# Optimization experiments

Hardware: AMD Instinct MI355X
Metric: run time of the kernel (lower is better)

The kernel has to match this reference:

```python
import jax, jax.numpy as jnp
import numpy as np

N_NODES = 50000
N_EDGES = 800000
D = 256          # node / edge feature dim (hs[-1])
H = 512          # hs[0] == hs[1] == 2*D
LN_EPS = 1e-5


def setup_inputs() -> dict:
    key = jax.random.key(0)
    ks = jax.random.split(key, 8)
    x = jax.random.normal(ks[0], (N_NODES, D), dtype=jnp.float32)
    edge_index = jax.random.randint(ks[1], (2, N_EDGES), 0, N_NODES, dtype=jnp.int64)
    edge_attr = jax.random.normal(ks[2], (N_EDGES, D), dtype=jnp.float32)
    # MLP(hs=[512,512,256]): Linear(512->512) + SiLU, Linear(512->256); then LayerNorm(256)
    s1 = 1.0 / np.sqrt(H)
    s2 = 1.0 / np.sqrt(H)
    W1 = jax.random.uniform(ks[3], (H, H), jnp.float32, -s1, s1)
    b1 = jax.random.uniform(ks[4], (H,), jnp.float32, -s1, s1)
    W2 = jax.random.uniform(ks[5], (H, D), jnp.float32, -s2, s2)
    b2 = jax.random.uniform(ks[6], (D,), jnp.float32, -s2, s2)
    gamma = jnp.ones((D,), jnp.float32)
    beta = jnp.zeros((D,), jnp.float32)
    return {"x": x, "edge_index": edge_index, "edge_attr": edge_attr,
            "W1": W1, "b1": b1, "W2": W2, "b2": b2,
            "gamma": gamma, "beta": beta}


def reference(x, edge_index, edge_attr, W1, b1, W2, b2, gamma, beta):
    i = edge_index[0]  # destination nodes
    # scatter-add edge features onto nodes: [N, D]
    agg = jax.ops.segment_sum(edge_attr, i, num_segments=x.shape[0])
    h = jnp.concatenate([x, agg], axis=-1)            # [N, 2D]
    h = jax.nn.silu(h @ W1 + b1)                      # [N, H]
    h = h @ W2 + b2                                   # [N, D]
    # LayerNorm(D)
    mu = jnp.mean(h, axis=-1, keepdims=True)
    var = jnp.mean(jnp.square(h - mu), axis=-1, keepdims=True)
    h = (h - mu) * jax.lax.rsqrt(var + LN_EPS) * gamma + beta
    return h + x
```

## Files before the change

kernel.cpp:

```cpp
#include <hip/hip_runtime.h>
#include <hip/hip_bf16.h>
#include <math.h>
#include <stdint.h>

typedef __bf16 bf16_t;
typedef __bf16 bf16x4 __attribute__((ext_vector_type(4)));
typedef __bf16 bf16x8 __attribute__((ext_vector_type(8)));
typedef float  f32x4  __attribute__((ext_vector_type(4)));

#define D_FEAT 256
#define H_FEAT 512
#define LN_EPS 1e-5f
#define CAP    96

#define GLOBAL_AS __attribute__((address_space(1)))
#define LDS_AS    __attribute__((address_space(3)))

__global__ __launch_bounds__(256) void wprep_kernel(const float* __restrict__ W1,
                                                    const float* __restrict__ W2,
                                                    bf16_t* __restrict__ W1t,
                                                    bf16_t* __restrict__ W2t,
                                                    int* __restrict__ counts, int n_nodes) {
    __shared__ float tile[32][33];
    int b = blockIdx.x;
    int gtid = b * 256 + threadIdx.x;
    if (gtid < n_nodes) counts[gtid] = 0;

    int tx = threadIdx.x & 31, ty = threadIdx.x >> 5;
    if (b < 256) {
        int k0 = (b >> 4) * 32, n0 = (b & 15) * 32;
#pragma unroll
        for (int j = 0; j < 4; ++j)
            tile[ty * 4 + j][tx] = W1[(size_t)(k0 + ty * 4 + j) * H_FEAT + n0 + tx];
        __syncthreads();
#pragma unroll
        for (int j = 0; j < 4; ++j)
            W1t[(size_t)(n0 + ty * 4 + j) * H_FEAT + k0 + tx] = (bf16_t)tile[tx][ty * 4 + j];
    } else {
        int bb = b - 256;
        int k0 = (bb >> 3) * 32, n0 = (bb & 7) * 32;
#pragma unroll
        for (int j = 0; j < 4; ++j)
            tile[ty * 4 + j][tx] = W2[(size_t)(k0 + ty * 4 + j) * D_FEAT + n0 + tx];
        __syncthreads();
#pragma unroll
        for (int j = 0; j < 4; ++j)
            W2t[(size_t)(n0 + ty * 4 + j) * H_FEAT + k0 + tx] = (bf16_t)tile[tx][ty * 4 + j];
    }
}

__global__ void place_kernel(const int* __restrict__ dst, int* __restrict__ counts,
                             int* __restrict__ sorted_eid, int n_edges) {
    int e = blockIdx.x * blockDim.x + threadIdx.x;
    if (e < n_edges) {
        int d = dst[e];
        int pos = atomicAdd(&counts[d], 1);
        if (pos < CAP) sorted_eid[(long)d * CAP + pos] = e;
    }
}

__global__ __launch_bounds__(256) void gather_kernel(
    const float* __restrict__ edge_attr, const int* __restrict__ sorted_eid,
    const int* __restrict__ counts, const float* __restrict__ x,
    bf16_t* __restrict__ h_in, int n_nodes) {
    int node = (blockIdx.x * blockDim.x + threadIdx.x) >> 6;
    int lane = threadIdx.x & 63;
    if (node >= n_nodes) return;
    int cnt_all = counts[node]; if (cnt_all > CAP) cnt_all = CAP;
    long s = (long)node * CAP;

    f32x4 accA = {0.f, 0.f, 0.f, 0.f};
    f32x4 accB = {0.f, 0.f, 0.f, 0.f};
    for (int b0 = 0; b0 < cnt_all; b0 += 64) {
        int cnt = cnt_all - b0; if (cnt > 64) cnt = 64;
        int eid_l = (b0 + lane < cnt_all) ? sorted_eid[s + b0 + lane] : 0;
        int j = 0;
        for (; j + 4 <= cnt; j += 4) {
            int e0 = __shfl(eid_l, j);
            int e1 = __shfl(eid_l, j + 1);
            int e2 = __shfl(eid_l, j + 2);
            int e3 = __shfl(eid_l, j + 3);
            f32x4 v0 = __builtin_nontemporal_load((const f32x4*)(edge_attr + (long)e0 * D_FEAT + lane * 4));
            f32x4 v1 = __builtin_nontemporal_load((const f32x4*)(edge_attr + (long)e1 * D_FEAT + lane * 4));
            f32x4 v2 = __builtin_nontemporal_load((const f32x4*)(edge_attr + (long)e2 * D_FEAT + lane * 4));
            f32x4 v3 = __builtin_nontemporal_load((const f32x4*)(edge_attr + (long)e3 * D_FEAT + lane * 4));
            accA += v0; accB += v1; accA += v2; accB += v3;
        }
        for (; j < cnt; ++j) {
            int e0 = __shfl(eid_l, j);
            accA += __builtin_nontemporal_load((const f32x4*)(edge_attr + (long)e0 * D_FEAT + lane * 4));
        }
    }
    f32x4 acc = accA + accB;

    const f32x4 xv = *(const f32x4*)(x + (long)node * D_FEAT + lane * 4);
    bf16x4 ox, oa;
#pragma unroll
    for (int i = 0; i < 4; ++i) { ox[i] = (bf16_t)xv[i]; oa[i] = (bf16_t)acc[i]; }
    *(bf16x4*)(h_in + (long)node * H_FEAT + lane * 4) = ox;
    *(bf16x4*)(h_in + (long)node * H_FEAT + D_FEAT + lane * 4) = oa;
}

__global__ __launch_bounds__(256) void gemm1_kernel(
    const bf16_t* __restrict__ h_in, const bf16_t* __restrict__ W1t,
    const float* __restrict__ b1, bf16_t* __restrict__ act, int n_nodes) {
    __shared__ bf16_t As[2][128 * 32];
    __shared__ bf16_t Bs[2][128 * 32];
    int l = threadIdx.x & 63;
    int w = threadIdx.x >> 6;
    int wr = w >> 1, wc = w & 1;
    int browbase = blockIdx.x * 128;
    int bcolbase = blockIdx.y * 128;
    int lr = l & 15;
    int sg = l >> 4;

    f32x4 zero = {0.f, 0.f, 0.f, 0.f};
    f32x4 acc[4][4];
#pragma unroll
    for (int m = 0; m < 4; ++m)
#pragma unroll
        for (int n = 0; n < 4; ++n) acc[m][n] = zero;

    auto stage = [&](int buf, int k0) {
#pragma unroll
        for (int q = 0; q < 2; ++q) {
            int lrow = w * 32 + q * 16 + (l >> 2);
            int ssrc = (l & 3) ^ ((lrow >> 1) & 3);
            int ga = browbase + lrow; if (ga >= n_nodes) ga = 0;
            const bf16_t* gA = h_in + (size_t)ga * H_FEAT + k0 + ssrc * 8;
            bf16_t* lA = &As[buf][(w * 32 + q * 16) * 32];
            __builtin_amdgcn_global_load_lds((const GLOBAL_AS uint32_t*)gA,
                                             (LDS_AS uint32_t*)lA, 16, 0, 0);
            int gb = bcolbase + lrow;
            const bf16_t* gB = W1t + (size_t)gb * H_FEAT + k0 + ssrc * 8;
            bf16_t* lB = &Bs[buf][(w * 32 + q * 16) * 32];
            __builtin_amdgcn_global_load_lds((const GLOBAL_AS uint32_t*)gB,
                                             (LDS_AS uint32_t*)lB, 16, 0, 0);
        }
    };

    stage(0, 0);
    __syncthreads();
    int cur = 0;
    for (int t = 0; t < 16; ++t) {
        if (t < 15) stage(cur ^ 1, (t + 1) * 32);
        bf16x8 a[4], b[4];
#pragma unroll
        for (int m = 0; m < 4; ++m) {
            int row = wr * 64 + m * 16 + lr;
            int s = sg ^ ((row >> 1) & 3);
            a[m] = *(const bf16x8*)&As[cur][row * 32 + s * 8];
        }
#pragma unroll
        for (int n = 0; n < 4; ++n) {
            int col = wc * 64 + n * 16 + lr;
            int s = sg ^ ((col >> 1) & 3);
            b[n] = *(const bf16x8*)&Bs[cur][col * 32 + s * 8];
        }
#pragma unroll
        for (int m = 0; m < 4; ++m)
#pragma unroll
            for (int n = 0; n < 4; ++n)
                acc[m][n] = __builtin_amdgcn_mfma_f32_16x16x32_bf16(a[m], b[n], acc[m][n], 0, 0, 0);
        __syncthreads();
        cur ^= 1;
    }

    int rg = (l >> 4) * 4;
#pragma unroll
    for (int m = 0; m < 4; ++m) {
#pragma unroll
        for (int i = 0; i < 4; ++i) {
            int r = browbase + wr * 64 + m * 16 + rg + i;
            if (r >= n_nodes) continue;
#pragma unroll
            for (int n = 0; n < 4; ++n) {
                int c = bcolbase + wc * 64 + n * 16 + lr;
                float v = acc[m][n][i] + b1[c];
                v = v / (1.0f + __expf(-v));
                act[(long)r * H_FEAT + c] = (bf16_t)v;
            }
        }
    }
}

__global__ __launch_bounds__(256) void gemm2_ln_kernel(
    const bf16_t* __restrict__ act, const bf16_t* __restrict__ W2t,
    const float* __restrict__ b2, const float* __restrict__ gamma,
    const float* __restrict__ beta, const float* __restrict__ x,
    float* __restrict__ out, int n_nodes) {
    __shared__ bf16_t As[2][64 * 32];
    __shared__ bf16_t Bs[2][256 * 32];
    int tid = threadIdx.x;
    int l = tid & 63, w = tid >> 6;
    int lr = l & 15, sg = l >> 4;
    int brow = blockIdx.x * 64;

    int a_row = tid >> 2;
    int a_ssrc = (tid & 3) ^ ((a_row >> 1) & 3);
    int a_node = brow + a_row; if (a_node >= n_nodes) a_node = 0;

    f32x4 zero = {0.f, 0.f, 0.f, 0.f};
    f32x4 acc[16];
#pragma unroll
    for (int n = 0; n < 16; ++n) acc[n] = zero;

    auto stage = [&](int buf, int k0) {
        {
            const bf16_t* src = act + (size_t)a_node * H_FEAT + k0 + a_ssrc * 8;
            bf16_t* dst = &As[buf][w * 512];
            __builtin_amdgcn_global_load_lds((const GLOBAL_AS uint32_t*)src,
                                             (LDS_AS uint32_t*)dst, 16, 0, 0);
        }
#pragma unroll
        for (int q = 0; q < 4; ++q) {
            int e = q * 256 + tid;
            int r = e >> 2;
            int ssrc = (e & 3) ^ ((r >> 1) & 3);
            const bf16_t* src = W2t + (size_t)r * H_FEAT + k0 + ssrc * 8;
            bf16_t* dst = &Bs[buf][q * 2048 + w * 512];
            __builtin_amdgcn_global_load_lds((const GLOBAL_AS uint32_t*)src,
                                             (LDS_AS uint32_t*)dst, 16, 0, 0);
        }
    };

    stage(0, 0);
    __syncthreads();
    int cur = 0;
    for (int t = 0; t < 16; ++t) {
        if (t < 15) stage(cur ^ 1, (t + 1) * 32);
        int arow = w * 16 + lr;
        bf16x8 a = *(const bf16x8*)&As[cur][arow * 32 + (sg ^ ((arow >> 1) & 3)) * 8];
#pragma unroll
        for (int n = 0; n < 16; ++n) {
            int bcol = n * 16 + lr;
            bf16x8 b = *(const bf16x8*)&Bs[cur][bcol * 32 + (sg ^ ((bcol >> 1) & 3)) * 8];
            acc[n] = __builtin_amdgcn_mfma_f32_16x16x32_bf16(a, b, acc[n], 0, 0, 0);
        }
        __syncthreads();
        cur ^= 1;
    }

#pragma unroll
    for (int n = 0; n < 16; ++n) {
        float bb = b2[n * 16 + lr];
#pragma unroll
        for (int i = 0; i < 4; ++i) acc[n][i] += bb;
    }

    float s[4] = {0.f, 0.f, 0.f, 0.f};
    float q[4] = {0.f, 0.f, 0.f, 0.f};
#pragma unroll
    for (int n = 0; n < 16; ++n)
#pragma unroll
        for (int i = 0; i < 4; ++i) {
            float v = acc[n][i];
            s[i] += v;
            q[i] += v * v;
        }
#pragma unroll
    for (int m = 1; m < 16; m <<= 1) {
#pragma unroll
        for (int i = 0; i < 4; ++i) {
            s[i] += __shfl_xor(s[i], m);
            q[i] += __shfl_xor(q[i], m);
        }
    }
    float mu[4], rstd[4];
#pragma unroll
    for (int i = 0; i < 4; ++i) {
        mu[i] = s[i] * (1.0f / 256.0f);
        float var = q[i] * (1.0f / 256.0f) - mu[i] * mu[i];
        rstd[i] = rsqrtf(var + LN_EPS);
    }

    int rg = sg * 4;
#pragma unroll
    for (int n = 0; n < 16; ++n) {
        int c2 = n * 16 + lr;
        float g = gamma[c2], bt = beta[c2];
#pragma unroll
        for (int i = 0; i < 4; ++i) {
            int r = brow + w * 16 + rg + i;
            if (r >= n_nodes) continue;
            float v = (acc[n][i] - mu[i]) * rstd[i] * g + bt + x[(long)r * D_FEAT + c2];
            out[(long)r * D_FEAT + c2] = v;
        }
    }
}

extern "C" void kernel_launch(void* const* d_in, const int* in_sizes, int n_in,
                              void* d_out, int out_size, void* d_ws, size_t ws_size,
                              hipStream_t stream) {
    const float* x         = (const float*)d_in[0];
    const int*   edge_idx  = (const int*)d_in[1];
    const float* edge_attr = (const float*)d_in[2];
    const float* W1        = (const float*)d_in[3];
    const float* b1        = (const float*)d_in[4];
    const float* W2        = (const float*)d_in[5];
    const float* b2        = (const float*)d_in[6];
    const float* gamma     = (const float*)d_in[7];
    const float* beta      = (const float*)d_in[8];
    float* out = (float*)d_out;

    int n_nodes = in_sizes[0] / D_FEAT;
    int n_edges = in_sizes[2] / D_FEAT;

    char* ws = (char*)d_ws;
    size_t off = 0;
    bf16_t* h_in   = (bf16_t*)(ws + off); off += (size_t)n_nodes * H_FEAT * 2;
    bf16_t* act    = (bf16_t*)(ws + off); off += (size_t)n_nodes * H_FEAT * 2;
    bf16_t* W1t    = (bf16_t*)(ws + off); off += (size_t)H_FEAT * H_FEAT * 2;
    bf16_t* W2t    = (bf16_t*)(ws + off); off += (size_t)D_FEAT * H_FEAT * 2;
    int* counts    = (int*)(ws + off);    off += (size_t)n_nodes * 4;
    int* sorted_eid= (int*)(ws + off);    off += (size_t)n_nodes * CAP * 4;

    wprep_kernel<<<384, 256, 0, stream>>>(W1, W2, W1t, W2t, counts, n_nodes);

    place_kernel<<<(n_edges + 255) / 256, 256, 0, stream>>>(edge_idx, counts, sorted_eid, n_edges);

    {
        int blocks = (n_nodes * 64 + 255) / 256;
        gather_kernel<<<blocks, 256, 0, stream>>>(edge_attr, sorted_eid, counts, x, h_in, n_nodes);
    }

    {
        dim3 grid((n_nodes + 127) / 128, H_FEAT / 128);
        gemm1_kernel<<<grid, 256, 0, stream>>>(h_in, W1t, b1, act, n_nodes);
    }

    {
        int blocks = (n_nodes + 63) / 64;
        gemm2_ln_kernel<<<blocks, 256, 0, stream>>>(act, W2t, b2, gamma, beta, x, out, n_nodes);
    }
}
```

Measured before the change: 345.8 us.

## Enlarge gemm1 tile to 128x256 with 512 threads and XCD-aware block remap

GEMM1 now runs 512-thread blocks that each compute a 128x256 output tile instead of 128x128, so every A tile loaded from h_in is reused across twice as many columns. The grid becomes 1D and block IDs are remapped so consecutive logical tiles, which share A rows, land on the same XCD for better L2 locality. Loading is restructured to match: one A load and two B loads per thread per stage. The trade-off is more LDS per block (48KB) and fewer blocks, which may lower occupancy.

```diff
diff --git a/kernel.cpp b/kernel.cpp
--- a/kernel.cpp
+++ b/kernel.cpp
@@ -101,18 +101,27 @@
     *(bf16x4*)(h_in + (long)node * H_FEAT + D_FEAT + lane * 4) = oa;
 }
 
-__global__ __launch_bounds__(256) void gemm1_kernel(
+__global__ __launch_bounds__(512) void gemm1_kernel(
     const bf16_t* __restrict__ h_in, const bf16_t* __restrict__ W1t,
     const float* __restrict__ b1, bf16_t* __restrict__ act, int n_nodes) {
     __shared__ bf16_t As[2][128 * 32];
-    __shared__ bf16_t Bs[2][128 * 32];
-    int l = threadIdx.x & 63;
-    int w = threadIdx.x >> 6;
-    int wr = w >> 1, wc = w & 1;
-    int browbase = blockIdx.x * 128;
-    int bcolbase = blockIdx.y * 128;
-    int lr = l & 15;
-    int sg = l >> 4;
+    __shared__ bf16_t Bs[2][256 * 32];
+    int tid = threadIdx.x;
+    int l = tid & 63, w = tid >> 6;
+    int wr = w >> 2, wc = w & 3;
+    int lr = l & 15, sg = l >> 4;
+
+    int nwg = gridDim.x;
+    int orig = blockIdx.x;
+    int q = nwg >> 3, r = nwg & 7;
+    int xcd = orig & 7, within = orig >> 3;
+    int wgid = (xcd < r ? xcd * (q + 1) : r * (q + 1) + (xcd - r) * q) + within;
+    int browbase = (wgid >> 1) * 128;
+    int bcolbase = (wgid & 1) * 256;
+
+    int a_row = tid >> 2;
+    int a_ssrc = (tid & 3) ^ ((a_row >> 1) & 3);
+    int a_node = browbase + a_row; if (a_node >= n_nodes) a_node = 0;
 
     f32x4 zero = {0.f, 0.f, 0.f, 0.f};
     f32x4 acc[4][4];
@@ -122,20 +131,21 @@
         for (int n = 0; n < 4; ++n) acc[m][n] = zero;
 
     auto stage = [&](int buf, int k0) {
-#pragma unroll
-        for (int q = 0; q < 2; ++q) {
-            int lrow = w * 32 + q * 16 + (l >> 2);
-            int ssrc = (l & 3) ^ ((lrow >> 1) & 3);
-            int ga = browbase + lrow; if (ga >= n_nodes) ga = 0;
-            const bf16_t* gA = h_in + (size_t)ga * H_FEAT + k0 + ssrc * 8;
-            bf16_t* lA = &As[buf][(w * 32 + q * 16) * 32];
-            __builtin_amdgcn_global_load_lds((const GLOBAL_AS uint32_t*)gA,
-                                             (LDS_AS uint32_t*)lA, 16, 0, 0);
-            int gb = bcolbase + lrow;
-            const bf16_t* gB = W1t + (size_t)gb * H_FEAT + k0 + ssrc * 8;
-            bf16_t* lB = &Bs[buf][(w * 32 + q * 16) * 32];
-            __builtin_amdgcn_global_load_lds((const GLOBAL_AS uint32_t*)gB,
-                                             (LDS_AS uint32_t*)lB, 16, 0, 0);
+        {
+            const bf16_t* src = h_in + (size_t)a_node * H_FEAT + k0 + a_ssrc * 8;
+            bf16_t* dst = &As[buf][w * 512];
+            __builtin_amdgcn_global_load_lds((const GLOBAL_AS uint32_t*)src,
+                                             (LDS_AS uint32_t*)dst, 16, 0, 0);
+        }
+#pragma unroll
+        for (int qq = 0; qq < 2; ++qq) {
+            int e = qq * 512 + tid;
+            int rrow = e >> 2;
+            int ssrc = (e & 3) ^ ((rrow >> 1) & 3);
+            const bf16_t* src = W1t + (size_t)(bcolbase + rrow) * H_FEAT + k0 + ssrc * 8;
+            bf16_t* dst = &Bs[buf][qq * 4096 + w * 512];
+            __builtin_amdgcn_global_load_lds((const GLOBAL_AS uint32_t*)src,
+                                             (LDS_AS uint32_t*)dst, 16, 0, 0);
         }
     };
 
@@ -166,19 +176,19 @@
         cur ^= 1;
     }
 
-    int rg = (l >> 4) * 4;
+    int rg = sg * 4;
 #pragma unroll
     for (int m = 0; m < 4; ++m) {
 #pragma unroll
         for (int i = 0; i < 4; ++i) {
-            int r = browbase + wr * 64 + m * 16 + rg + i;
-            if (r >= n_nodes) continue;
+            int rr = browbase + wr * 64 + m * 16 + rg + i;
+            if (rr >= n_nodes) continue;
 #pragma unroll
             for (int n = 0; n < 4; ++n) {
                 int c = bcolbase + wc * 64 + n * 16 + lr;
                 float v = acc[m][n][i] + b1[c];
                 v = v / (1.0f + __expf(-v));
-                act[(long)r * H_FEAT + c] = (bf16_t)v;
+                act[(long)rr * H_FEAT + c] = (bf16_t)v;
             }
         }
     }
@@ -213,12 +223,12 @@
                                              (LDS_AS uint32_t*)dst, 16, 0, 0);
         }
 #pragma unroll
-        for (int q = 0; q < 4; ++q) {
-            int e = q * 256 + tid;
-            int r = e >> 2;
-            int ssrc = (e & 3) ^ ((r >> 1) & 3);
-            const bf16_t* src = W2t + (size_t)r * H_FEAT + k0 + ssrc * 8;
-            bf16_t* dst = &Bs[buf][q * 2048 + w * 512];
+        for (int qq = 0; qq < 4; ++qq) {
+            int e = qq * 256 + tid;
+            int rr = e >> 2;
+            int ssrc = (e & 3) ^ ((rr >> 1) & 3);
+            const bf16_t* src = W2t + (size_t)rr * H_FEAT + k0 + ssrc * 8;
+            bf16_t* dst = &Bs[buf][qq * 2048 + w * 512];
             __builtin_amdgcn_global_load_lds((const GLOBAL_AS uint32_t*)src,
                                              (LDS_AS uint32_t*)dst, 16, 0, 0);
         }
@@ -281,10 +291,10 @@
         float g = gamma[c2], bt = beta[c2];
 #pragma unroll
         for (int i = 0; i < 4; ++i) {
-            int r = brow + w * 16 + rg + i;
-            if (r >= n_nodes) continue;
-            float v = (acc[n][i] - mu[i]) * rstd[i] * g + bt + x[(long)r * D_FEAT + c2];
-            out[(long)r * D_FEAT + c2] = v;
+            int rr = brow + w * 16 + rg + i;
+            if (rr >= n_nodes) continue;
+            float v = (acc[n][i] - mu[i]) * rstd[i] * g + bt + x[(long)rr * D_FEAT + c2];
+            out[(long)rr * D_FEAT + c2] = v;
         }
     }
 }
@@ -325,8 +335,8 @@
     }
 
     {
-        dim3 grid((n_nodes + 127) / 128, H_FEAT / 128);
-        gemm1_kernel<<<grid, 256, 0, stream>>>(h_in, W1t, b1, act, n_nodes);
+        int nrow = (n_nodes + 127) / 128;
+        gemm1_kernel<<<nrow * 2, 512, 0, stream>>>(h_in, W1t, b1, act, n_nodes);
     }
 
     {
```

New measurement: 356.6 us. 3.1% more time.
